# Kernel optimization log

Measured on AMD Instinct MI355X. Metric: run time of the kernel, lower is better.

## Reference

```python
import jax, jax.numpy as jnp
import numpy as np

EPSILON = 1e-8
DT = 0.1
STEPS = 3
MASK_DENSITY = 0.01


def setup_inputs() -> dict:
    key = jax.random.key(0)
    k1, k2 = jax.random.split(key)
    B, S, D = 4, 4096, 2
    psi = jax.random.normal(k1, (B, S, D), dtype=jnp.float32)
    # binary mask: threshold a uniform draw to get a sparse 0/1 adjacency
    u = jax.random.uniform(k2, (B, S, S), dtype=jnp.float32)
    binary_mask = (u < MASK_DENSITY).astype(jnp.float32)
    return {"psi": psi, "binary_mask": binary_mask}


def reference(psi, binary_mask):
    def force(state):
        # adjacency-weighted aggregation minus self: [B,S,S] @ [B,S,2]
        return jnp.einsum('bij,bjd->bid', binary_mask, state) - state

    def step(p, _):
        r = jnp.linalg.norm(p, axis=-1, keepdims=True)          # [B,S,1]
        k1 = force(p)
        psi_star = p + DT * k1
        star_norm = jnp.linalg.norm(psi_star, axis=-1, keepdims=True)
        psi_star = psi_star * (r / (star_norm + EPSILON))       # renormalize to r
        k2 = force(psi_star)
        p_new = p + 0.5 * DT * (k1 + k2)
        new_norm = jnp.linalg.norm(p_new, axis=-1, keepdims=True)
        p_new = p_new * (r / (new_norm + EPSILON))              # norm-preserving
        return p_new, None

    psi_out, _ = jax.lax.scan(step, psi, None, length=STEPS)
    return psi_out
```

## Files before the change

kernel.cpp:

```cpp
#include <hip/hip_runtime.h>
#include <stdint.h>

#define BATCH   4
#define SEQ     4096
#define NROWS   (BATCH * SEQ)
#define SLOTS   80
#define SENT    SEQ
#define PSTR    4224
#define DTS     0.1f
#define HALF_DT 0.05f
#define EPS     1e-8f

__device__ __forceinline__ float2 ballot_force_sum(unsigned long long w,
                                                   const float2* __restrict__ gb,
                                                   int lane) {
    const int colbase = ((lane >> 2) << 8) | (lane & 3);
    float sx = 0.f, sy = 0.f;
    while (w) {
        int j = __builtin_ctzll(w);
        w &= (w - 1);
        float2 v = gb[colbase + (j << 2)];
        sx += v.x; sy += v.y;
    }
#pragma unroll
    for (int m = 32; m >= 1; m >>= 1) {
        sx += __shfl_xor(sx, m, 64);
        sy += __shfl_xor(sy, m, 64);
    }
    return make_float2(sx, sy);
}

__global__ __launch_bounds__(256)
void compress_phaseA(const float* __restrict__ mask,
                     const float2* __restrict__ psi,
                     unsigned int* __restrict__ idx,
                     float2* __restrict__ k1buf,
                     float2* __restrict__ star,
                     float2* __restrict__ pbuf,
                     float*  __restrict__ rbuf) {
    const int row  = (blockIdx.x * blockDim.x + threadIdx.x) >> 6;
    const int lane = threadIdx.x & 63;

    const float4* src = reinterpret_cast<const float4*>(mask + (size_t)row * SEQ);
    unsigned long long word = 0ull;
#pragma unroll
    for (int c = 0; c < 16; ++c) {
        float4 v = src[c * 64 + lane];
        unsigned long long b;
        b = __ballot(v.x != 0.f); if (lane == c * 4 + 0) word = b;
        b = __ballot(v.y != 0.f); if (lane == c * 4 + 1) word = b;
        b = __ballot(v.z != 0.f); if (lane == c * 4 + 2) word = b;
        b = __ballot(v.w != 0.f); if (lane == c * 4 + 3) word = b;
    }

    int pc  = __popcll(word);
    int inc = pc;
#pragma unroll
    for (int ofs = 1; ofs < 64; ofs <<= 1) {
        int t = __shfl_up(inc, ofs, 64);
        if (lane >= ofs) inc += t;
    }
    int pos   = inc - pc;
    int total = __shfl(inc, 63, 64);

    unsigned int* dst = idx + (size_t)row * SLOTS;
    const int colbase = ((lane >> 2) << 8) | (lane & 3);
    unsigned long long w = word;
    while (w) {
        int j = __builtin_ctzll(w);
        w &= (w - 1);
        if (pos < SLOTS) dst[pos] = (unsigned int)(colbase + (j << 2));
        ++pos;
    }
    for (int s = total + lane; s < SLOTS; s += 64) dst[s] = SENT;

    const int bidx = row >> 12;
    const int rloc = row & 4095;
    float2 sum = ballot_force_sum(word, psi + ((size_t)bidx << 12), lane);
    float2 p  = psi[row];
    float r   = sqrtf(p.x * p.x + p.y * p.y);
    float k1x = sum.x - p.x, k1y = sum.y - p.y;
    float tx  = p.x + DTS * k1x, ty = p.y + DTS * k1y;
    float sc  = r / (sqrtf(tx * tx + ty * ty) + EPS);
    if (lane == 0) {
        k1buf[row] = make_float2(k1x, k1y);
        rbuf[row]  = r;
        star[(size_t)bidx * PSTR + rloc] = make_float2(tx * sc, ty * sc);
        if (rloc == 0) {
            star[(size_t)bidx * PSTR + SENT] = make_float2(0.f, 0.f);
            pbuf[(size_t)bidx * PSTR + SENT] = make_float2(0.f, 0.f);
        }
    }
}

template <int PHASE>
__global__ __launch_bounds__(256)
void force_step(const unsigned int* __restrict__ idx,
                const float2* __restrict__ pIn, int pinStr,
                const float2* __restrict__ gath,
                float2* __restrict__ k1buf,
                float*  __restrict__ rbuf,
                float2* __restrict__ outbuf, int outStr) {
    const int tid  = blockIdx.x * blockDim.x + threadIdx.x;
    const int row  = tid >> 4;
    const int q    = tid & 15;
    const int bidx = row >> 12;
    const int rloc = row & 4095;
    const float2* __restrict__ gb = gath + (size_t)bidx * PSTR;

    const unsigned int* __restrict__ ip = idx + (size_t)row * SLOTS;

    float2 p = pIn[(size_t)bidx * pinStr + rloc];
    float2 st = make_float2(0.f, 0.f), k1 = make_float2(0.f, 0.f);
    float  rv = 0.f;
    if (PHASE == 1) { st = gb[rloc]; k1 = k1buf[row]; rv = rbuf[row]; }

    unsigned int c[5];
#pragma unroll
    for (int r = 0; r < 5; ++r) c[r] = ip[q * 5 + r];
    float sx = 0.f, sy = 0.f;
#pragma unroll
    for (int r = 0; r < 5; ++r) {
        float2 v = gb[c[r]];
        sx += v.x; sy += v.y;
    }
#pragma unroll
    for (int m = 8; m >= 1; m >>= 1) {
        sx += __shfl_xor(sx, m, 64);
        sy += __shfl_xor(sy, m, 64);
    }

    if (q == 0) {
        if (PHASE == 0) {
            float r   = sqrtf(p.x * p.x + p.y * p.y);
            float k1x = sx - p.x, k1y = sy - p.y;
            float tx  = p.x + DTS * k1x, ty = p.y + DTS * k1y;
            float sc  = r / (sqrtf(tx * tx + ty * ty) + EPS);
            k1buf[row] = make_float2(k1x, k1y);
            rbuf[row]  = r;
            outbuf[(size_t)bidx * outStr + rloc] = make_float2(tx * sc, ty * sc);
        } else {
            float k2x = sx - st.x, k2y = sy - st.y;
            float nx  = p.x + HALF_DT * (k1.x + k2x);
            float ny  = p.y + HALF_DT * (k1.y + k2y);
            float sc  = rv / (sqrtf(nx * nx + ny * ny) + EPS);
            outbuf[(size_t)bidx * outStr + rloc] = make_float2(nx * sc, ny * sc);
        }
    }
}

extern "C" void kernel_launch(void* const* d_in, const int* in_sizes, int n_in,
                              void* d_out, int out_size, void* d_ws, size_t ws_size,
                              hipStream_t stream) {
    const float* psi  = (const float*)d_in[0];
    const float* mask = (const float*)d_in[1];
    float2* out2 = (float2*)d_out;

    char* ws = (char*)d_ws;
    unsigned int* idx = (unsigned int*)ws;
    float2* pbuf = (float2*)(ws + (size_t)NROWS * SLOTS * sizeof(unsigned int));
    float2* star = pbuf + (size_t)BATCH * PSTR;
    float2* k1   = star + (size_t)BATCH * PSTR;
    float*  rbuf = (float*)(k1 + NROWS);

    const float2* psi2 = (const float2*)psi;

    compress_phaseA<<<NROWS / 4, 256, 0, stream>>>(mask, psi2, idx, k1, star, pbuf, rbuf);
    force_step<1><<<NROWS / 16, 256, 0, stream>>>(idx, psi2, SEQ, star, k1, rbuf, pbuf, PSTR);
    force_step<0><<<NROWS / 16, 256, 0, stream>>>(idx, pbuf, PSTR, pbuf, k1, rbuf, star, PSTR);
    force_step<1><<<NROWS / 16, 256, 0, stream>>>(idx, pbuf, PSTR, star, k1, rbuf, pbuf, PSTR);
    force_step<0><<<NROWS / 16, 256, 0, stream>>>(idx, pbuf, PSTR, pbuf, k1, rbuf, star, PSTR);
    force_step<1><<<NROWS / 16, 256, 0, stream>>>(idx, pbuf, PSTR, star, k1, rbuf, out2, SEQ);
}
```

Measured before the change: 380.3 us.

## Stage gather vector in LDS, shrink column indices to 16-bit, nontemporal mask loads

Each force_step block now copies the whole per-batch state vector (4096 float2) into shared memory and gathers neighbours from LDS instead of global memory. Column indices are stored as ushort, halving index traffic. Mask reads in the compress kernel use nontemporal loads so the mask does not pollute the cache. The cost is 32KB of redundant global-to-LDS copying per 256-thread block (only 16 rows per block) plus a barrier, which may outweigh the gather savings.

```diff
diff --git a/kernel.cpp b/kernel.cpp
--- a/kernel.cpp
+++ b/kernel.cpp
@@ -10,6 +10,8 @@
 #define DTS     0.1f
 #define HALF_DT 0.05f
 #define EPS     1e-8f
+
+typedef float fx4 __attribute__((ext_vector_type(4)));
 
 __device__ __forceinline__ float2 ballot_force_sum(unsigned long long w,
                                                    const float2* __restrict__ gb,
@@ -33,7 +35,7 @@
 __global__ __launch_bounds__(256)
 void compress_phaseA(const float* __restrict__ mask,
                      const float2* __restrict__ psi,
-                     unsigned int* __restrict__ idx,
+                     ushort* __restrict__ idx,
                      float2* __restrict__ k1buf,
                      float2* __restrict__ star,
                      float2* __restrict__ pbuf,
@@ -41,11 +43,11 @@
     const int row  = (blockIdx.x * blockDim.x + threadIdx.x) >> 6;
     const int lane = threadIdx.x & 63;
 
-    const float4* src = reinterpret_cast<const float4*>(mask + (size_t)row * SEQ);
+    const fx4* src = reinterpret_cast<const fx4*>(mask + (size_t)row * SEQ);
     unsigned long long word = 0ull;
 #pragma unroll
     for (int c = 0; c < 16; ++c) {
-        float4 v = src[c * 64 + lane];
+        fx4 v = __builtin_nontemporal_load(&src[c * 64 + lane]);
         unsigned long long b;
         b = __ballot(v.x != 0.f); if (lane == c * 4 + 0) word = b;
         b = __ballot(v.y != 0.f); if (lane == c * 4 + 1) word = b;
@@ -63,16 +65,16 @@
     int pos   = inc - pc;
     int total = __shfl(inc, 63, 64);
 
-    unsigned int* dst = idx + (size_t)row * SLOTS;
+    ushort* dst = idx + (size_t)row * SLOTS;
     const int colbase = ((lane >> 2) << 8) | (lane & 3);
     unsigned long long w = word;
     while (w) {
         int j = __builtin_ctzll(w);
         w &= (w - 1);
-        if (pos < SLOTS) dst[pos] = (unsigned int)(colbase + (j << 2));
+        if (pos < SLOTS) dst[pos] = (ushort)(colbase + (j << 2));
         ++pos;
     }
-    for (int s = total + lane; s < SLOTS; s += 64) dst[s] = SENT;
+    for (int s = total + lane; s < SLOTS; s += 64) dst[s] = (ushort)SENT;
 
     const int bidx = row >> 12;
     const int rloc = row & 4095;
@@ -95,12 +97,13 @@
 
 template <int PHASE>
 __global__ __launch_bounds__(256)
-void force_step(const unsigned int* __restrict__ idx,
+void force_step(const ushort* __restrict__ idx,
                 const float2* __restrict__ pIn, int pinStr,
                 const float2* __restrict__ gath,
                 float2* __restrict__ k1buf,
                 float*  __restrict__ rbuf,
                 float2* __restrict__ outbuf, int outStr) {
+    __shared__ float2 lds[SEQ + 2];
     const int tid  = blockIdx.x * blockDim.x + threadIdx.x;
     const int row  = tid >> 4;
     const int q    = tid & 15;
@@ -108,20 +111,33 @@
     const int rloc = row & 4095;
     const float2* __restrict__ gb = gath + (size_t)bidx * PSTR;
 
-    const unsigned int* __restrict__ ip = idx + (size_t)row * SLOTS;
+    {
+        const float4* __restrict__ g4 = reinterpret_cast<const float4*>(gb);
+        float4* l4 = reinterpret_cast<float4*>(lds);
+#pragma unroll
+        for (int t = 0; t < 8; ++t)
+            l4[threadIdx.x + t * 256] = g4[threadIdx.x + t * 256];
+        if (threadIdx.x == 0) lds[SENT] = gb[SENT];
+    }
 
-    float2 p = pIn[(size_t)bidx * pinStr + rloc];
-    float2 st = make_float2(0.f, 0.f), k1 = make_float2(0.f, 0.f);
-    float  rv = 0.f;
-    if (PHASE == 1) { st = gb[rloc]; k1 = k1buf[row]; rv = rbuf[row]; }
-
-    unsigned int c[5];
+    const ushort* __restrict__ ip = idx + (size_t)row * SLOTS;
+    int c[5];
 #pragma unroll
     for (int r = 0; r < 5; ++r) c[r] = ip[q * 5 + r];
+    float2 pg = make_float2(0.f, 0.f), k1 = make_float2(0.f, 0.f);
+    float  rv = 0.f;
+    if (PHASE == 1) {
+        pg = pIn[(size_t)bidx * pinStr + rloc];
+        k1 = k1buf[row];
+        rv = rbuf[row];
+    }
+
+    __syncthreads();
+
     float sx = 0.f, sy = 0.f;
 #pragma unroll
     for (int r = 0; r < 5; ++r) {
-        float2 v = gb[c[r]];
+        float2 v = lds[c[r]];
         sx += v.x; sy += v.y;
     }
 #pragma unroll
@@ -132,6 +148,7 @@
 
     if (q == 0) {
         if (PHASE == 0) {
+            float2 p  = lds[rloc];
             float r   = sqrtf(p.x * p.x + p.y * p.y);
             float k1x = sx - p.x, k1y = sy - p.y;
             float tx  = p.x + DTS * k1x, ty = p.y + DTS * k1y;
@@ -140,9 +157,10 @@
             rbuf[row]  = r;
             outbuf[(size_t)bidx * outStr + rloc] = make_float2(tx * sc, ty * sc);
         } else {
+            float2 st = lds[rloc];
             float k2x = sx - st.x, k2y = sy - st.y;
-            float nx  = p.x + HALF_DT * (k1.x + k2x);
-            float ny  = p.y + HALF_DT * (k1.y + k2y);
+            float nx  = pg.x + HALF_DT * (k1.x + k2x);
+            float ny  = pg.y + HALF_DT * (k1.y + k2y);
             float sc  = rv / (sqrtf(nx * nx + ny * ny) + EPS);
             outbuf[(size_t)bidx * outStr + rloc] = make_float2(nx * sc, ny * sc);
         }
@@ -157,8 +175,8 @@
     float2* out2 = (float2*)d_out;
 
     char* ws = (char*)d_ws;
-    unsigned int* idx = (unsigned int*)ws;
-    float2* pbuf = (float2*)(ws + (size_t)NROWS * SLOTS * sizeof(unsigned int));
+    ushort* idx = (ushort*)ws;
+    float2* pbuf = (float2*)(ws + (size_t)NROWS * SLOTS * sizeof(ushort));
     float2* star = pbuf + (size_t)BATCH * PSTR;
     float2* k1   = star + (size_t)BATCH * PSTR;
     float*  rbuf = (float*)(k1 + NROWS);
```

After: 355.5 us. -6.5%, faster.
